# Performance work log

Measured on AMD Instinct MI355X. Metric: run time of the kernel, lower is better.

## Reference

```python
import jax, jax.numpy as jnp
import numpy as np

D = 768  # input_hidden_dim
H = 768  # TGLU_hidden_dim
E = 128  # num_entity
B = 32   # batch_size
S = 128  # max_seq_len
LN_EPS = 1e-5


def setup_inputs() -> dict:
    key = jax.random.key(0)
    ks = jax.random.split(key, 14)
    sc = 1.0 / np.sqrt(D)
    return {
        "entity_text_cls": jax.random.normal(ks[0], (E, D), jnp.float32),
        "entity_text_tokens": jax.random.normal(ks[1], (E, S, D), jnp.float32),
        "mention_text_cls": jax.random.normal(ks[2], (B, D), jnp.float32),
        "mention_text_tokens": jax.random.normal(ks[3], (B, S, D), jnp.float32),
        "Wq": jax.random.normal(ks[4], (D, H), jnp.float32) * sc,
        "bq": jax.random.normal(ks[5], (H,), jnp.float32) * 0.02,
        "Wk": jax.random.normal(ks[6], (D, H), jnp.float32) * sc,
        "bk": jax.random.normal(ks[7], (H,), jnp.float32) * 0.02,
        "Wv": jax.random.normal(ks[8], (D, H), jnp.float32) * sc,
        "bv": jax.random.normal(ks[9], (H,), jnp.float32) * 0.02,
        "Wc": jax.random.normal(ks[10], (D, H), jnp.float32) * sc,
        "bc": jax.random.normal(ks[11], (H,), jnp.float32) * 0.02,
        "ln_g": jnp.ones((H,), jnp.float32),
        "ln_b": jnp.zeros((H,), jnp.float32),
    }


def reference(entity_text_cls, entity_text_tokens, mention_text_cls, mention_text_tokens,
              Wq, bq, Wk, bk, Wv, bv, Wc, bc, ln_g, ln_b):
    # projections
    cls_fc = entity_text_cls @ Wc + bc                     # [E, H]
    q = entity_text_tokens @ Wq + bq                       # [E, S, H]
    k = mention_text_tokens @ Wk + bk                      # [B, S, H]
    v = mention_text_tokens @ Wv + bv                      # [B, S, H]
    # broadcast cross attention: every entity attends to every mention
    scale = 1.0 / jnp.sqrt(jnp.asarray(H, q.dtype))
    scores = jnp.einsum('esh,bth->ebst', q, k) * scale     # [E, B, S, S]
    probs = jax.nn.softmax(scores, axis=-1)                # [E, B, S, S]
    # context = mean over query positions of probs @ v  -> fuse mean into einsum
    seq = jnp.asarray(q.shape[1], q.dtype)
    ctx = jnp.einsum('ebst,bth->ebh', probs, v) / seq      # [E, B, H]
    # layernorm over H
    mu = jnp.mean(ctx, axis=-1, keepdims=True)
    var = jnp.mean(jnp.square(ctx - mu), axis=-1, keepdims=True)
    ctx_ln = (ctx - mu) * jax.lax.rsqrt(var + LN_EPS) * ln_g + ln_b
    # dual matching scores
    g2l = jnp.einsum('eh,ebh->eb', cls_fc, ctx_ln).T       # [B, E]
    g2g = mention_text_cls @ entity_text_cls.T             # [B, E]
    return (g2l + g2g) * 0.5
```

## Files before the change

### kernel.cpp

```cpp
#include <hip/hip_runtime.h>

typedef unsigned short u16;
typedef __bf16 bf16x8 __attribute__((ext_vector_type(8)));
typedef float f32x4 __attribute__((ext_vector_type(4)));
typedef u16 u16x8 __attribute__((ext_vector_type(8)));
typedef u16 u16x4 __attribute__((ext_vector_type(4)));

static __device__ __forceinline__ u16 f2bf(float x){
  unsigned u = __float_as_uint(x);
  u += 0x7fffu + ((u >> 16) & 1u);
  return (u16)(u >> 16);
}
static __device__ __forceinline__ float bf2f(u16 u){
  return __uint_as_float(((unsigned)u) << 16);
}

#define MFMA __builtin_amdgcn_mfma_f32_16x16x32_bf16

#define GLD1(GP, LP) __builtin_amdgcn_global_load_lds( \
    (const __attribute__((address_space(1))) unsigned int*)(GP), \
    (__attribute__((address_space(3))) unsigned int*)(LP), 16, 0, 0)

#define DECL_ACC \
  f32x4 acc00={},acc01={},acc02={},acc03={}, \
        acc10={},acc11={},acc12={},acc13={}, \
        acc20={},acc21={},acc22={},acc23={}, \
        acc30={},acc31={},acc32={},acc33={};

#define CORE_SETUP \
  int tid = threadIdx.x; \
  int lane = tid & 63, w = tid >> 6; \
  int wm = (w >> 1) * 64, wn = (w & 1) * 64; \
  int quad = lane >> 4, l16 = lane & 15; \
  int r8 = lane >> 3, c8 = lane & 7; \
  int p0 = quad ^ (l16 & 7); \
  const u16* Agl = Ablk + (size_t)(w*32 + r8)*KS + (size_t)((c8 ^ r8)*8); \
  const u16* Bgl = Bblk + (size_t)(w*32 + r8)*KS + (size_t)((c8 ^ r8)*8); \
  u16* sAl = sA + w*2048; \
  u16* sBl = sB + w*2048; \
  const u16* paA0 = sA + (wm + l16)*64 + p0*8; \
  const u16* paA1 = sA + (wm + l16)*64 + (p0^4)*8; \
  const u16* paB0 = sB + (wn + l16)*64 + p0*8; \
  const u16* paB1 = sB + (wn + l16)*64 + (p0^4)*8;

#define GLDS8(K0) do { \
  const u16* ga_ = Agl + (K0); \
  const u16* gb_ = Bgl + (K0); \
  GLD1(ga_,         sAl);        GLD1(ga_ +  8*KS, sAl +  512); \
  GLD1(ga_ + 16*KS, sAl + 1024); GLD1(ga_ + 24*KS, sAl + 1536); \
  GLD1(gb_,         sBl);        GLD1(gb_ +  8*KS, sBl +  512); \
  GLD1(gb_ + 16*KS, sBl + 1024); GLD1(gb_ + 24*KS, sBl + 1536); \
} while(0)

#define KKSTEP(PA, PB) do { \
  bf16x8 a0 = *(const bf16x8*)(PA); \
  bf16x8 a1 = *(const bf16x8*)((PA) + 1024); \
  bf16x8 a2 = *(const bf16x8*)((PA) + 2048); \
  bf16x8 a3 = *(const bf16x8*)((PA) + 3072); \
  bf16x8 b0 = *(const bf16x8*)(PB); \
  bf16x8 b1 = *(const bf16x8*)((PB) + 1024); \
  bf16x8 b2 = *(const bf16x8*)((PB) + 2048); \
  bf16x8 b3 = *(const bf16x8*)((PB) + 3072); \
  acc00 = MFMA(a0,b0,acc00,0,0,0); acc01 = MFMA(a0,b1,acc01,0,0,0); \
  acc02 = MFMA(a0,b2,acc02,0,0,0); acc03 = MFMA(a0,b3,acc03,0,0,0); \
  acc10 = MFMA(a1,b0,acc10,0,0,0); acc11 = MFMA(a1,b1,acc11,0,0,0); \
  acc12 = MFMA(a1,b2,acc12,0,0,0); acc13 = MFMA(a1,b3,acc13,0,0,0); \
  acc20 = MFMA(a2,b0,acc20,0,0,0); acc21 = MFMA(a2,b1,acc21,0,0,0); \
  acc22 = MFMA(a2,b2,acc22,0,0,0); acc23 = MFMA(a2,b3,acc23,0,0,0); \
  acc30 = MFMA(a3,b0,acc30,0,0,0); acc31 = MFMA(a3,b1,acc31,0,0,0); \
  acc32 = MFMA(a3,b2,acc32,0,0,0); acc33 = MFMA(a3,b3,acc33,0,0,0); \
} while(0)

#define KLOOP do { \
  for (int k0 = 0; k0 < KLEN; k0 += 64){ \
    __syncthreads(); \
    GLDS8(k0); \
    __syncthreads(); \
    KKSTEP(paA0, paB0); \
    KKSTEP(paA1, paB1); \
  } } while(0)

template<int KLEN, int KS, bool TRANSC>
static __device__ __forceinline__ void gemm128_core(
    const u16* __restrict__ Ablk, const u16* __restrict__ Bblk,
    const float* __restrict__ bias, u16* __restrict__ C,
    int mb, int nb, u16* sA, u16* sB)
{
  CORE_SETUP
  DECL_ACC
  KLOOP;
  int cb = nb*128 + wn + l16;
  float bb0=0.f, bb1=0.f, bb2=0.f, bb3=0.f;
  if (bias){ bb0=bias[cb]; bb1=bias[cb+16]; bb2=bias[cb+32]; bb3=bias[cb+48]; }
  if constexpr (!TRANSC) {
#define GEPI(IM,A0,A1,A2,A3) do { \
  int r0_ = mb*128 + wm + (IM)*16 + quad*4; \
  _Pragma("unroll") \
  for (int j=0;j<4;j++){ \
    C[(size_t)(r0_+j)*768 + cb     ] = f2bf(A0[j]+bb0); \
    C[(size_t)(r0_+j)*768 + cb + 16] = f2bf(A1[j]+bb1); \
    C[(size_t)(r0_+j)*768 + cb + 32] = f2bf(A2[j]+bb2); \
    C[(size_t)(r0_+j)*768 + cb + 48] = f2bf(A3[j]+bb3); \
  } } while(0)
    GEPI(0, acc00,acc01,acc02,acc03);
    GEPI(1, acc10,acc11,acc12,acc13);
    GEPI(2, acc20,acc21,acc22,acc23);
    GEPI(3, acc30,acc31,acc32,acc33);
#undef GEPI
  } else {
#define GEPT(IM,A0,A1,A2,A3) do { \
  int t0_ = wm + (IM)*16 + quad*4; \
  u16x4 p0_ = {f2bf(A0[0]+bb0),f2bf(A0[1]+bb0),f2bf(A0[2]+bb0),f2bf(A0[3]+bb0)}; \
  u16x4 p1_ = {f2bf(A1[0]+bb1),f2bf(A1[1]+bb1),f2bf(A1[2]+bb1),f2bf(A1[3]+bb1)}; \
  u16x4 p2_ = {f2bf(A2[0]+bb2),f2bf(A2[1]+bb2),f2bf(A2[2]+bb2),f2bf(A2[3]+bb2)}; \
  u16x4 p3_ = {f2bf(A3[0]+bb3),f2bf(A3[1]+bb3),f2bf(A3[2]+bb3),f2bf(A3[3]+bb3)}; \
  *(u16x4*)(C + (size_t)(cb     )*128 + t0_) = p0_; \
  *(u16x4*)(C + (size_t)(cb + 16)*128 + t0_) = p1_; \
  *(u16x4*)(C + (size_t)(cb + 32)*128 + t0_) = p2_; \
  *(u16x4*)(C + (size_t)(cb + 48)*128 + t0_) = p3_; \
} while(0)
    GEPT(0, acc00,acc01,acc02,acc03);
    GEPT(1, acc10,acc11,acc12,acc13);
    GEPT(2, acc20,acc21,acc22,acc23);
    GEPT(3, acc30,acc31,acc32,acc33);
#undef GEPT
  }
}

__global__ __launch_bounds__(256) void prep(
    const float* __restrict__ etok, u16* __restrict__ entb,
    const float* __restrict__ mtok, u16* __restrict__ menb,
    const float* __restrict__ ecls, u16* __restrict__ eclsb,
    const float* __restrict__ Wv, const float* __restrict__ Wc,
    u16* __restrict__ wvt, u16* __restrict__ wct,
    const float* __restrict__ Wq, const float* __restrict__ Wk,
    u16* __restrict__ mtb,
    const float* __restrict__ bq, const float* __restrict__ bk,
    float* __restrict__ wrb, float* __restrict__ c2b)
{
  __shared__ __align__(16) u16 shm[2*128*72];
  int blk = blockIdx.x;
  int tid = threadIdx.x;
  if (blk < 36){
    int mbq = blk/6, nbq = blk%6;
    u16* tA = shm; u16* tB = shm + 128*72;
    int lane = tid & 63, w = tid >> 6;
    int wm = (w >> 1) * 64, wn = (w & 1) * 64;
    int quad = lane >> 4, l16 = lane & 15;
    int sr = tid >> 3, sc = (tid & 7) * 8;
    const float* Ag = Wq + (size_t)(mbq*128+sr)*768 + sc;
    const float* Bg = Wk + (size_t)(nbq*128+sr)*768 + sc;
    u16* tAp = tA + sr*72 + sc;
    u16* tBp = tB + sr*72 + sc;
    DECL_ACC
    for (int k0=0;k0<768;k0+=64){
      __syncthreads();
#define STG(G) do { \
      float4 xa0=*(const float4*)(Ag+(G)*32*768+k0), xa1=*(const float4*)(Ag+(G)*32*768+k0+4); \
      float4 xb0=*(const float4*)(Bg+(G)*32*768+k0), xb1=*(const float4*)(Bg+(G)*32*768+k0+4); \
      u16x8 ra={f2bf(xa0.x),f2bf(xa0.y),f2bf(xa0.z),f2bf(xa0.w), \
                f2bf(xa1.x),f2bf(xa1.y),f2bf(xa1.z),f2bf(xa1.w)}; \
      u16x8 rb={f2bf(xb0.x),f2bf(xb0.y),f2bf(xb0.z),f2bf(xb0.w), \
                f2bf(xb1.x),f2bf(xb1.y),f2bf(xb1.z),f2bf(xb1.w)}; \
      *(u16x8*)(tAp+(G)*32*72)=ra; *(u16x8*)(tBp+(G)*32*72)=rb; \
      } while(0)
      STG(0); STG(1); STG(2); STG(3);
#undef STG
      __syncthreads();
#define KK72(KB) do { \
      const u16* pa_=tA+(wm+l16)*72+(KB)+quad*8; \
      const u16* pb_=tB+(wn+l16)*72+(KB)+quad*8; \
      bf16x8 a0=*(const bf16x8*)(pa_),      a1=*(const bf16x8*)(pa_+16*72); \
      bf16x8 a2=*(const bf16x8*)(pa_+32*72),a3=*(const bf16x8*)(pa_+48*72); \
      bf16x8 b0=*(const bf16x8*)(pb_),      b1=*(const bf16x8*)(pb_+16*72); \
      bf16x8 b2=*(const bf16x8*)(pb_+32*72),b3=*(const bf16x8*)(pb_+48*72); \
      acc00=MFMA(a0,b0,acc00,0,0,0); acc01=MFMA(a0,b1,acc01,0,0,0); \
      acc02=MFMA(a0,b2,acc02,0,0,0); acc03=MFMA(a0,b3,acc03,0,0,0); \
      acc10=MFMA(a1,b0,acc10,0,0,0); acc11=MFMA(a1,b1,acc11,0,0,0); \
      acc12=MFMA(a1,b2,acc12,0,0,0); acc13=MFMA(a1,b3,acc13,0,0,0); \
      acc20=MFMA(a2,b0,acc20,0,0,0); acc21=MFMA(a2,b1,acc21,0,0,0); \
      acc22=MFMA(a2,b2,acc22,0,0,0); acc23=MFMA(a2,b3,acc23,0,0,0); \
      acc30=MFMA(a3,b0,acc30,0,0,0); acc31=MFMA(a3,b1,acc31,0,0,0); \
      acc32=MFMA(a3,b2,acc32,0,0,0); acc33=MFMA(a3,b3,acc33,0,0,0); \
      } while(0)
      KK72(0); KK72(32);
#undef KK72
    }
    int cb = nbq*128 + wn + l16;
#define GEPM(IM,A0,A1,A2,A3) do { \
    int r0_ = mbq*128 + wm + (IM)*16 + quad*4; \
    _Pragma("unroll") \
    for (int j=0;j<4;j++){ \
      mtb[(size_t)(r0_+j)*768 + cb     ] = f2bf(A0[j]); \
      mtb[(size_t)(r0_+j)*768 + cb + 16] = f2bf(A1[j]); \
      mtb[(size_t)(r0_+j)*768 + cb + 32] = f2bf(A2[j]); \
      mtb[(size_t)(r0_+j)*768 + cb + 48] = f2bf(A3[j]); \
    } } while(0)
    GEPM(0, acc00,acc01,acc02,acc03);
    GEPM(1, acc10,acc11,acc12,acc13);
    GEPM(2, acc20,acc21,acc22,acc23);
    GEPM(3, acc30,acc31,acc32,acc33);
#undef GEPM
  } else if (blk < 48){
    int n = blk - 36;
    const float* M; const float* v; float* o;
    int j;
    if (n < 6){ M=Wk; v=bq; o=wrb; j=n; } else { M=Wq; v=bk; o=c2b; j=n-6; }
    int rr = tid >> 1, row = j*128 + rr;
    const float4* p = (const float4*)(M + (size_t)row*768 + (tid&1)*384);
    const float4* q = (const float4*)(v + (tid&1)*384);
    float s = 0.f;
    #pragma unroll 8
    for (int i=0;i<96;i++){
      float4 a=p[i], c=q[i];
      s += a.x*c.x + a.y*c.y + a.z*c.z + a.w*c.w;
    }
    s += __shfl_xor(s, 1);
    if (!(tid&1)) o[row] = s;
  } else if (blk == 48){
    float s = 0.f;
    for (int i=tid;i<768;i+=256) s += bk[i]*bq[i];
    #pragma unroll
    for (int d2=1; d2<64; d2<<=1) s += __shfl_xor(s,d2);
    float* red = (float*)shm;
    int lane = tid & 63, w = tid >> 6;
    if (lane==0) red[w]=s;
    __syncthreads();
    if (tid==0) wrb[768] = red[0]+red[1]+red[2]+red[3];
  } else if (blk < 7777){
    int i = (blk - 49) * 256 + tid;
    const float* s; u16* d; int off;
    if (i < 1572864)      { s=etok; d=entb; off=i; }
    else if (i < 1966080) { s=mtok; d=menb; off=i-1572864; }
    else                  { s=ecls; d=eclsb; off=i-1966080; }
    const float4* s4 = (const float4*)s;
    float4 a = s4[(size_t)off*2], b = s4[(size_t)off*2+1];
    u16x8 r;
    r[0]=f2bf(a.x); r[1]=f2bf(a.y); r[2]=f2bf(a.z); r[3]=f2bf(a.w);
    r[4]=f2bf(b.x); r[5]=f2bf(b.y); r[6]=f2bf(b.z); r[7]=f2bf(b.w);
    *(u16x8*)(d + (size_t)off*8) = r;
  } else {
    int n = blk - 7777;
    int z = n / 576, rem = n % 576;
    const float* s = z ? Wc : Wv;
    u16*         d = z ? wct : wvt;
    float* t = (float*)shm;
    int bx = (rem % 24) * 32, by = (rem / 24) * 32;
    int tx = tid & 31, ty = (tid >> 5) * 4;
    for (int i=0;i<4;i++)
      t[(ty+i)*33 + tx] = s[(size_t)(by+ty+i)*768 + bx+tx];
    __syncthreads();
    for (int i=0;i<4;i++)
      d[(size_t)(bx+ty+i)*768 + by+tx] = f2bf(t[tx*33 + ty+i]);
  }
}

__global__ __launch_bounds__(256, 1) void proj(
    const u16* __restrict__ men, const u16* __restrict__ eclsb,
    const u16* __restrict__ wvt, const u16* __restrict__ wct,
    const u16* __restrict__ mtb,
    const float* __restrict__ bv, const float* __restrict__ bc,
    const float* __restrict__ c2b, const float* __restrict__ wrb,
    u16* __restrict__ vtb, u16* __restrict__ gtb, u16* __restrict__ clsb,
    float* __restrict__ rbias)
{
  __shared__ __align__(16) u16 sA[128*64];
  __shared__ __align__(16) u16 sB[128*64];
  int y = blockIdx.y, mb = blockIdx.x;
  if (y < 6){
    gemm128_core<768,768,true>(men + (size_t)mb*128*768, wvt + (size_t)y*128*768,
                               bv, vtb + (size_t)mb*98304, mb, y, sA, sB);
  } else if (y < 12){
    gemm128_core<768,768,false>(men + (size_t)mb*128*768, mtb + (size_t)(y-6)*128*768,
                                c2b, gtb, mb, y-6, sA, sB);
  } else if (y == 12){
    if (mb >= 6) return;
    gemm128_core<768,768,false>(eclsb, wct + (size_t)mb*128*768, bc, clsb, 0, mb, sA, sB);
  } else {
    int tid = threadIdx.x;
    int rr = tid >> 1, row = mb*128 + rr;
    const u16* p = men + (size_t)row*768 + (tid&1)*384;
    const float* q = wrb + (tid&1)*384;
    float s = 0.f;
    #pragma unroll 8
    for (int i=0;i<48;i++){
      u16x8 v = *(const u16x8*)(p + i*8);
      s += bf2f(v[0])*q[i*8]   + bf2f(v[1])*q[i*8+1]
         + bf2f(v[2])*q[i*8+2] + bf2f(v[3])*q[i*8+3]
         + bf2f(v[4])*q[i*8+4] + bf2f(v[5])*q[i*8+5]
         + bf2f(v[6])*q[i*8+6] + bf2f(v[7])*q[i*8+7];
    }
    s += __shfl_xor(s, 1);
    if (!(tid&1)) rbias[row] = s + wrb[768];
  }
}

__global__ __launch_bounds__(256, 1) void attnk(
    const u16* __restrict__ ent, const u16* __restrict__ gt,
    const float* __restrict__ rbias, u16* __restrict__ ptbf)
{
  __shared__ __align__(16) u16 sA[128*64];
  __shared__ __align__(16) u16 sB[128*64];
  __shared__ float rbufA[256];
  __shared__ float rbufB[256];
  int bi = blockIdx.x;
  int b = bi >> 7, e = bi & 127;
  const u16* Ablk = ent + (size_t)e * 128 * 768;
  const u16* Bblk = gt  + (size_t)b * 128 * 768;
  constexpr int KS = 768;
  CORE_SETUP
  DECL_ACC
  int ph = (bi & 3) * 3;
  for (int it = 0; it < 12; it++){
    int kidx = it + ph; if (kidx >= 12) kidx -= 12;
    int k0 = kidx << 6;
    __syncthreads();
    GLDS8(k0);
    __syncthreads();
    KKSTEP(paA0, paB0);
    KKSTEP(paA1, paB1);
  }
  const float c1 = 0.036084391824351615f * 1.4426950408889634f;
  float rs0 = rbias[b*128 + wn      + l16] * c1;
  float rs1 = rbias[b*128 + wn + 16 + l16] * c1;
  float rs2 = rbias[b*128 + wn + 32 + l16] * c1;
  float rs3 = rbias[b*128 + wn + 48 + l16] * c1;
#define EXPSUM(IM,A0,A1,A2,A3) do { \
  _Pragma("unroll") \
  for (int j=0;j<4;j++){ \
    int r_ = wm + (IM)*16 + quad*4 + j; \
    float e0 = exp2f(fmaf(A0[j], c1, rs0)); \
    float e1 = exp2f(fmaf(A1[j], c1, rs1)); \
    float e2 = exp2f(fmaf(A2[j], c1, rs2)); \
    float e3 = exp2f(fmaf(A3[j], c1, rs3)); \
    A0[j]=e0; A1[j]=e1; A2[j]=e2; A3[j]=e3; \
    float s = (e0+e1)+(e2+e3); \
    s += __shfl_xor(s,1); s += __shfl_xor(s,2); \
    s += __shfl_xor(s,4); s += __shfl_xor(s,8); \
    if (l16==0) rbufB[(w&1)*128 + r_] = s; \
  } } while(0)
  EXPSUM(0, acc00,acc01,acc02,acc03);
  EXPSUM(1, acc10,acc11,acc12,acc13);
  EXPSUM(2, acc20,acc21,acc22,acc23);
  EXPSUM(3, acc30,acc31,acc32,acc33);
#undef EXPSUM
  __syncthreads();
  float csum0=0.f, csum1=0.f, csum2=0.f, csum3=0.f;
#define CSUM(IM,A0,A1,A2,A3) do { \
  _Pragma("unroll") \
  for (int j=0;j<4;j++){ \
    int r_ = wm + (IM)*16 + quad*4 + j; \
    float inv = __builtin_amdgcn_rcpf(rbufB[r_]+rbufB[128+r_]); \
    csum0 += A0[j]*inv; csum1 += A1[j]*inv; \
    csum2 += A2[j]*inv; csum3 += A3[j]*inv; \
  } } while(0)
  CSUM(0, acc00,acc01,acc02,acc03);
  CSUM(1, acc10,acc11,acc12,acc13);
  CSUM(2, acc20,acc21,acc22,acc23);
  CSUM(3, acc30,acc31,acc32,acc33);
#undef CSUM
  csum0 += __shfl_xor(csum0,16); csum0 += __shfl_xor(csum0,32);
  csum1 += __shfl_xor(csum1,16); csum1 += __shfl_xor(csum1,32);
  csum2 += __shfl_xor(csum2,16); csum2 += __shfl_xor(csum2,32);
  csum3 += __shfl_xor(csum3,16); csum3 += __shfl_xor(csum3,32);
  if (quad == 0){
    rbufA[(w>>1)*128 + wn      + l16] = csum0;
    rbufA[(w>>1)*128 + wn + 16 + l16] = csum1;
    rbufA[(w>>1)*128 + wn + 32 + l16] = csum2;
    rbufA[(w>>1)*128 + wn + 48 + l16] = csum3;
  }
  __syncthreads();
  if (tid < 128)
    ptbf[((size_t)b*128 + e)*128 + tid] =
        f2bf((rbufA[tid] + rbufA[128+tid]) * 0.0078125f);
}

__global__ __launch_bounds__(256, 1) void ctx2(
    const u16* __restrict__ ptbf, const u16* __restrict__ vtb,
    u16* __restrict__ ctxb)
{
  __shared__ __align__(16) u16 sA[128*64];
  __shared__ __align__(16) u16 sB[128*64];
  int b = blockIdx.y, nb = blockIdx.x;
  gemm128_core<128,128,false>(ptbf + (size_t)b*16384,
                              vtb + (size_t)b*98304 + (size_t)nb*16384,
                              nullptr, ctxb + (size_t)b*98304, 0, nb, sA, sB);
}

__global__ __launch_bounds__(256) void fin(
    const u16* __restrict__ ctxb, const u16* __restrict__ clsfc,
    const float* __restrict__ ecls, const float* __restrict__ mcls,
    const float* __restrict__ lng, const float* __restrict__ lnb,
    float* __restrict__ out)
{
  int bi = blockIdx.x;
  int b = bi >> 7, e = bi & 127;
  int tid = threadIdx.x;
  int lane = tid & 63, w = tid >> 6;
  __shared__ float redbuf[8];
  const u16* cr = ctxb + ((size_t)b*128 + e)*768;
  float a0 = bf2f(cr[tid]), a1 = bf2f(cr[tid+256]), a2 = bf2f(cr[tid+512]);
  float s1 = a0+a1+a2;
  float s2 = a0*a0 + a1*a1 + a2*a2;
  #pragma unroll
  for (int d2=1; d2<64; d2<<=1){ s1 += __shfl_xor(s1,d2); s2 += __shfl_xor(s2,d2); }
  if (lane==0){ redbuf[w]=s1; redbuf[4+w]=s2; }
  __syncthreads();
  s1 = redbuf[0]+redbuf[1]+redbuf[2]+redbuf[3];
  s2 = redbuf[4]+redbuf[5]+redbuf[6]+redbuf[7];
  float mu = s1 * (1.0f/768.0f);
  float var = s2 * (1.0f/768.0f) - mu*mu;
  float rstd = rsqrtf(var + 1e-5f);
  float dd = 0.f;
  {
    int h = tid;
    float y = (a0-mu)*rstd*lng[h] + lnb[h];
    dd += y * bf2f(clsfc[e*768+h]) + mcls[b*768+h]*ecls[e*768+h];
    h = tid + 256;
    y = (a1-mu)*rstd*lng[h] + lnb[h];
    dd += y * bf2f(clsfc[e*768+h]) + mcls[b*768+h]*ecls[e*768+h];
    h = tid + 512;
    y = (a2-mu)*rstd*lng[h] + lnb[h];
    dd += y * bf2f(clsfc[e*768+h]) + mcls[b*768+h]*ecls[e*768+h];
  }
  #pragma unroll
  for (int d2=1; d2<64; d2<<=1) dd += __shfl_xor(dd,d2);
  __syncthreads();
  if (lane==0) redbuf[w] = dd;
  __syncthreads();
  if (tid==0) out[bi] = 0.5f * (redbuf[0]+redbuf[1]+redbuf[2]+redbuf[3]);
}

extern "C" void kernel_launch(void* const* d_in, const int* in_sizes, int n_in,
                              void* d_out, int out_size, void* d_ws, size_t ws_size,
                              hipStream_t stream)
{
  (void)in_sizes; (void)n_in; (void)out_size; (void)ws_size;
  const float* ecls = (const float*)d_in[0];
  const float* etok = (const float*)d_in[1];
  const float* mcls = (const float*)d_in[2];
  const float* mtok = (const float*)d_in[3];
  const float* Wq   = (const float*)d_in[4];
  const float* bq   = (const float*)d_in[5];
  const float* Wk   = (const float*)d_in[6];
  const float* bk   = (const float*)d_in[7];
  const float* Wv   = (const float*)d_in[8];
  const float* bv   = (const float*)d_in[9];
  const float* Wc   = (const float*)d_in[10];
  const float* bc   = (const float*)d_in[11];
  const float* lng  = (const float*)d_in[12];
  const float* lnb  = (const float*)d_in[13];
  float* out = (float*)d_out;
  char* ws = (char*)d_ws;

  u16* ent_bf  = (u16*)(ws + 0);
  u16* men_bf  = (u16*)(ws + 25165824);
  u16* ecls_bf = (u16*)(ws + 31457280);
  u16* wvt     = (u16*)(ws + 31653888);
  u16* wct     = (u16*)(ws + 32833536);
  u16* mtb     = (u16*)(ws + 34013184);
  u16* vtb     = (u16*)(ws + 35192832);
  u16* clsb    = (u16*)(ws + 41484288);
  u16* gtb     = (u16*)(ws + 41680896);
  float* rbias = (float*)(ws + 47972352);
  float* wrb   = (float*)(ws + 47988736);
  float* c2b   = (float*)(ws + 47992832);
  u16* ptbf    = (u16*)(ws + 47996928);
  u16* ctxb    = (u16*)(ws + 49045504);

  prep<<<8929, 256, 0, stream>>>(etok, ent_bf, mtok, men_bf, ecls, ecls_bf,
                                 Wv, Wc, wvt, wct, Wq, Wk, mtb,
                                 bq, bk, wrb, c2b);
  proj<<<dim3(32,14), 256, 0, stream>>>(men_bf, ecls_bf, wvt, wct, mtb,
                                        bv, bc, c2b, wrb,
                                        vtb, gtb, clsb, rbias);
  attnk<<<4096, 256, 0, stream>>>(ent_bf, gtb, rbias, ptbf);
  ctx2<<<dim3(6,32), 256, 0, stream>>>(ptbf, vtb, ctxb);
  fin<<<4096, 256, 0, stream>>>(ctxb, clsb, ecls, mcls, lng, lnb, out);
}
```

Before: 299.1 us.

## Use FP8 operands and scaled MFMA for the attention score GEMM

Entity tokens and the folded query-key projection output are now stored as FP8 instead of bf16, and the score GEMM in the attention kernel uses the 16x16x128 FP8 scaled MFMA with 128-wide K tiles. This halves the bytes loaded for the dominant per-(entity, batch) GEMM and raises MFMA throughput per instruction. The cost is reduced precision in the softmax scores, which may affect accuracy against the reference, and the per-block K rotation phase is dropped.

```diff
diff --git a/kernel.cpp b/kernel.cpp
--- a/kernel.cpp
+++ b/kernel.cpp
@@ -1,10 +1,12 @@
 #include <hip/hip_runtime.h>
 
 typedef unsigned short u16;
+typedef unsigned char u8;
 typedef __bf16 bf16x8 __attribute__((ext_vector_type(8)));
 typedef float f32x4 __attribute__((ext_vector_type(4)));
 typedef u16 u16x8 __attribute__((ext_vector_type(8)));
 typedef u16 u16x4 __attribute__((ext_vector_type(4)));
+typedef int i32x8 __attribute__((ext_vector_type(8)));
 
 static __device__ __forceinline__ u16 f2bf(float x){
   unsigned u = __float_as_uint(x);
@@ -14,8 +16,14 @@
 static __device__ __forceinline__ float bf2f(u16 u){
   return __uint_as_float(((unsigned)u) << 16);
 }
+static __device__ __forceinline__ u8 f2fp8(float x){
+  int p = __builtin_amdgcn_cvt_pk_fp8_f32(x, x, 0, false);
+  return (u8)(p & 0xff);
+}
 
 #define MFMA __builtin_amdgcn_mfma_f32_16x16x32_bf16
+#define MFMA8(A,B,C) __builtin_amdgcn_mfma_scale_f32_16x16x128_f8f6f4( \
+    (A), (B), (C), 0, 0, 0, 0x7F7F7F7F, 0, 0x7F7F7F7F)
 
 #define GLD1(GP, LP) __builtin_amdgcn_global_load_lds( \
     (const __attribute__((address_space(1))) unsigned int*)(GP), \
@@ -80,10 +88,10 @@
     KKSTEP(paA1, paB1); \
   } } while(0)
 
-template<int KLEN, int KS, bool TRANSC>
+template<int KLEN, int KS, int OM>
 static __device__ __forceinline__ void gemm128_core(
     const u16* __restrict__ Ablk, const u16* __restrict__ Bblk,
-    const float* __restrict__ bias, u16* __restrict__ C,
+    const float* __restrict__ bias, void* __restrict__ Cv,
     int mb, int nb, u16* sA, u16* sB)
 {
   CORE_SETUP
@@ -92,7 +100,8 @@
   int cb = nb*128 + wn + l16;
   float bb0=0.f, bb1=0.f, bb2=0.f, bb3=0.f;
   if (bias){ bb0=bias[cb]; bb1=bias[cb+16]; bb2=bias[cb+32]; bb3=bias[cb+48]; }
-  if constexpr (!TRANSC) {
+  if constexpr (OM == 0) {
+    u16* C = (u16*)Cv;
 #define GEPI(IM,A0,A1,A2,A3) do { \
   int r0_ = mb*128 + wm + (IM)*16 + quad*4; \
   _Pragma("unroll") \
@@ -107,7 +116,8 @@
     GEPI(2, acc20,acc21,acc22,acc23);
     GEPI(3, acc30,acc31,acc32,acc33);
 #undef GEPI
-  } else {
+  } else if constexpr (OM == 1) {
+    u16* C = (u16*)Cv;
 #define GEPT(IM,A0,A1,A2,A3) do { \
   int t0_ = wm + (IM)*16 + quad*4; \
   u16x4 p0_ = {f2bf(A0[0]+bb0),f2bf(A0[1]+bb0),f2bf(A0[2]+bb0),f2bf(A0[3]+bb0)}; \
@@ -124,11 +134,27 @@
     GEPT(2, acc20,acc21,acc22,acc23);
     GEPT(3, acc30,acc31,acc32,acc33);
 #undef GEPT
+  } else {
+    u8* C = (u8*)Cv;
+#define GEP8(IM,A0,A1,A2,A3) do { \
+  int r0_ = mb*128 + wm + (IM)*16 + quad*4; \
+  _Pragma("unroll") \
+  for (int j=0;j<4;j++){ \
+    C[(size_t)(r0_+j)*768 + cb     ] = f2fp8(A0[j]+bb0); \
+    C[(size_t)(r0_+j)*768 + cb + 16] = f2fp8(A1[j]+bb1); \
+    C[(size_t)(r0_+j)*768 + cb + 32] = f2fp8(A2[j]+bb2); \
+    C[(size_t)(r0_+j)*768 + cb + 48] = f2fp8(A3[j]+bb3); \
+  } } while(0)
+    GEP8(0, acc00,acc01,acc02,acc03);
+    GEP8(1, acc10,acc11,acc12,acc13);
+    GEP8(2, acc20,acc21,acc22,acc23);
+    GEP8(3, acc30,acc31,acc32,acc33);
+#undef GEP8
   }
 }
 
 __global__ __launch_bounds__(256) void prep(
-    const float* __restrict__ etok, u16* __restrict__ entb,
+    const float* __restrict__ etok, u8* __restrict__ ent8,
     const float* __restrict__ mtok, u16* __restrict__ menb,
     const float* __restrict__ ecls, u16* __restrict__ eclsb,
     const float* __restrict__ Wv, const float* __restrict__ Wc,
@@ -229,16 +255,26 @@
     if (tid==0) wrb[768] = red[0]+red[1]+red[2]+red[3];
   } else if (blk < 7777){
     int i = (blk - 49) * 256 + tid;
-    const float* s; u16* d; int off;
-    if (i < 1572864)      { s=etok; d=entb; off=i; }
-    else if (i < 1966080) { s=mtok; d=menb; off=i-1572864; }
-    else                  { s=ecls; d=eclsb; off=i-1966080; }
-    const float4* s4 = (const float4*)s;
-    float4 a = s4[(size_t)off*2], b = s4[(size_t)off*2+1];
-    u16x8 r;
-    r[0]=f2bf(a.x); r[1]=f2bf(a.y); r[2]=f2bf(a.z); r[3]=f2bf(a.w);
-    r[4]=f2bf(b.x); r[5]=f2bf(b.y); r[6]=f2bf(b.z); r[7]=f2bf(b.w);
-    *(u16x8*)(d + (size_t)off*8) = r;
+    if (i < 1572864){
+      const float4* s4 = (const float4*)etok;
+      float4 a = s4[(size_t)i*2], b = s4[(size_t)i*2+1];
+      int d0 = __builtin_amdgcn_cvt_pk_fp8_f32(a.x, a.y, 0, false);
+      d0 = __builtin_amdgcn_cvt_pk_fp8_f32(a.z, a.w, d0, true);
+      int d1 = __builtin_amdgcn_cvt_pk_fp8_f32(b.x, b.y, 0, false);
+      d1 = __builtin_amdgcn_cvt_pk_fp8_f32(b.z, b.w, d1, true);
+      int2 r; r.x = d0; r.y = d1;
+      *(int2*)(ent8 + (size_t)i*8) = r;
+    } else {
+      const float* s; u16* d; int off;
+      if (i < 1966080) { s=mtok; d=menb; off=i-1572864; }
+      else             { s=ecls; d=eclsb; off=i-1966080; }
+      const float4* s4 = (const float4*)s;
+      float4 a = s4[(size_t)off*2], b = s4[(size_t)off*2+1];
+      u16x8 r;
+      r[0]=f2bf(a.x); r[1]=f2bf(a.y); r[2]=f2bf(a.z); r[3]=f2bf(a.w);
+      r[4]=f2bf(b.x); r[5]=f2bf(b.y); r[6]=f2bf(b.z); r[7]=f2bf(b.w);
+      *(u16x8*)(d + (size_t)off*8) = r;
+    }
   } else {
     int n = blk - 7777;
     int z = n / 576, rem = n % 576;
@@ -261,21 +297,21 @@
     const u16* __restrict__ mtb,
     const float* __restrict__ bv, const float* __restrict__ bc,
     const float* __restrict__ c2b, const float* __restrict__ wrb,
-    u16* __restrict__ vtb, u16* __restrict__ gtb, u16* __restrict__ clsb,
+    u16* __restrict__ vtb, u8* __restrict__ gt8, u16* __restrict__ clsb,
     float* __restrict__ rbias)
 {
   __shared__ __align__(16) u16 sA[128*64];
   __shared__ __align__(16) u16 sB[128*64];
   int y = blockIdx.y, mb = blockIdx.x;
   if (y < 6){
-    gemm128_core<768,768,true>(men + (size_t)mb*128*768, wvt + (size_t)y*128*768,
-                               bv, vtb + (size_t)mb*98304, mb, y, sA, sB);
+    gemm128_core<768,768,1>(men + (size_t)mb*128*768, wvt + (size_t)y*128*768,
+                            bv, vtb + (size_t)mb*98304, mb, y, sA, sB);
   } else if (y < 12){
-    gemm128_core<768,768,false>(men + (size_t)mb*128*768, mtb + (size_t)(y-6)*128*768,
-                                c2b, gtb, mb, y-6, sA, sB);
+    gemm128_core<768,768,2>(men + (size_t)mb*128*768, mtb + (size_t)(y-6)*128*768,
+                            c2b, gt8, mb, y-6, sA, sB);
   } else if (y == 12){
     if (mb >= 6) return;
-    gemm128_core<768,768,false>(eclsb, wct + (size_t)mb*128*768, bc, clsb, 0, mb, sA, sB);
+    gemm128_core<768,768,0>(eclsb, wct + (size_t)mb*128*768, bc, clsb, 0, mb, sA, sB);
   } else {
     int tid = threadIdx.x;
     int rr = tid >> 1, row = mb*128 + rr;
@@ -296,30 +332,73 @@
 }
 
 __global__ __launch_bounds__(256, 1) void attnk(
-    const u16* __restrict__ ent, const u16* __restrict__ gt,
+    const u8* __restrict__ ent, const u8* __restrict__ gt,
     const float* __restrict__ rbias, u16* __restrict__ ptbf)
 {
-  __shared__ __align__(16) u16 sA[128*64];
-  __shared__ __align__(16) u16 sB[128*64];
+  __shared__ __align__(16) u8 sA[128*128];
+  __shared__ __align__(16) u8 sB[128*128];
   __shared__ float rbufA[256];
   __shared__ float rbufB[256];
   int bi = blockIdx.x;
   int b = bi >> 7, e = bi & 127;
-  const u16* Ablk = ent + (size_t)e * 128 * 768;
-  const u16* Bblk = gt  + (size_t)b * 128 * 768;
-  constexpr int KS = 768;
-  CORE_SETUP
+  const u8* Ablk = ent + (size_t)e * 128 * 768;
+  const u8* Bblk = gt  + (size_t)b * 128 * 768;
+  int tid = threadIdx.x;
+  int lane = tid & 63, w = tid >> 6;
+  int wm = (w >> 1) * 64, wn = (w & 1) * 64;
+  int quad = lane >> 4, l16 = lane & 15;
+  int r8 = lane >> 3, c8 = lane & 7;
+  const u8* Agl = Ablk + (size_t)(w*32 + r8)*768 + (size_t)((c8 ^ r8)*16);
+  const u8* Bgl = Bblk + (size_t)(w*32 + r8)*768 + (size_t)((c8 ^ r8)*16);
+  u8* sAl = sA + w*4096;
+  u8* sBl = sB + w*4096;
+  int rb = l16 & 7;
+  const u8* paA0 = sA + (wm + l16)*128 + (((quad*2  )^rb)*16);
+  const u8* paA1 = sA + (wm + l16)*128 + (((quad*2+1)^rb)*16);
+  const u8* paB0 = sB + (wn + l16)*128 + (((quad*2  )^rb)*16);
+  const u8* paB1 = sB + (wn + l16)*128 + (((quad*2+1)^rb)*16);
   DECL_ACC
-  int ph = (bi & 3) * 3;
-  for (int it = 0; it < 12; it++){
-    int kidx = it + ph; if (kidx >= 12) kidx -= 12;
-    int k0 = kidx << 6;
+#define LDI(V, P0, P1) i32x8 V; { \
+  uint4 lo_ = *(const uint4*)(P0); uint4 hi_ = *(const uint4*)(P1); \
+  V = (i32x8){(int)lo_.x,(int)lo_.y,(int)lo_.z,(int)lo_.w, \
+              (int)hi_.x,(int)hi_.y,(int)hi_.z,(int)hi_.w}; }
+  for (int k0 = 0; k0 < 768; k0 += 128){
     __syncthreads();
-    GLDS8(k0);
+    {
+      const u8* ga_ = Agl + k0;
+      const u8* gb_ = Bgl + k0;
+      GLD1(ga_,          sAl);        GLD1(ga_ +  8*768, sAl + 1024);
+      GLD1(ga_ + 16*768, sAl + 2048); GLD1(ga_ + 24*768, sAl + 3072);
+      GLD1(gb_,          sBl);        GLD1(gb_ +  8*768, sBl + 1024);
+      GLD1(gb_ + 16*768, sBl + 2048); GLD1(gb_ + 24*768, sBl + 3072);
+    }
     __syncthreads();
-    KKSTEP(paA0, paB0);
-    KKSTEP(paA1, paB1);
+    LDI(b0, paB0,        paB1);
+    LDI(b1, paB0 + 2048, paB1 + 2048);
+    LDI(b2, paB0 + 4096, paB1 + 4096);
+    LDI(b3, paB0 + 6144, paB1 + 6144);
+    {
+      LDI(a_, paA0, paA1);
+      acc00=MFMA8(a_,b0,acc00); acc01=MFMA8(a_,b1,acc01);
+      acc02=MFMA8(a_,b2,acc02); acc03=MFMA8(a_,b3,acc03);
+    }
+    {
+      LDI(a_, paA0 + 2048, paA1 + 2048);
+      acc10=MFMA8(a_,b0,acc10); acc11=MFMA8(a_,b1,acc11);
+      acc12=MFMA8(a_,b2,acc12); acc13=MFMA8(a_,b3,acc13);
+    }
+    {
+      LDI(a_, paA0 + 4096, paA1 + 4096);
+      acc20=MFMA8(a_,b0,acc20); acc21=MFMA8(a_,b1,acc21);
+      acc22=MFMA8(a_,b2,acc22); acc23=MFMA8(a_,b3,acc23);
+    }
+    {
+      LDI(a_, paA0 + 6144, paA1 + 6144);
+      acc30=MFMA8(a_,b0,acc30); acc31=MFMA8(a_,b1,acc31);
+      acc32=MFMA8(a_,b2,acc32); acc33=MFMA8(a_,b3,acc33);
+    }
   }
+#undef LDI
   const float c1 = 0.036084391824351615f * 1.4426950408889634f;
   float rs0 = rbias[b*128 + wn      + l16] * c1;
   float rs1 = rbias[b*128 + wn + 16 + l16] * c1;
@@ -382,9 +461,9 @@
   __shared__ __align__(16) u16 sA[128*64];
   __shared__ __align__(16) u16 sB[128*64];
   int b = blockIdx.y, nb = blockIdx.x;
-  gemm128_core<128,128,false>(ptbf + (size_t)b*16384,
-                              vtb + (size_t)b*98304 + (size_t)nb*16384,
-                              nullptr, ctxb + (size_t)b*98304, 0, nb, sA, sB);
+  gemm128_core<128,128,0>(ptbf + (size_t)b*16384,
+                          vtb + (size_t)b*98304 + (size_t)nb*16384,
+                          nullptr, ctxb + (size_t)b*98304, 0, nb, sA, sB);
 }
 
 __global__ __launch_bounds__(256) void fin(
@@ -453,28 +532,28 @@
   float* out = (float*)d_out;
   char* ws = (char*)d_ws;
 
-  u16* ent_bf  = (u16*)(ws + 0);
-  u16* men_bf  = (u16*)(ws + 25165824);
-  u16* ecls_bf = (u16*)(ws + 31457280);
-  u16* wvt     = (u16*)(ws + 31653888);
-  u16* wct     = (u16*)(ws + 32833536);
-  u16* mtb     = (u16*)(ws + 34013184);
-  u16* vtb     = (u16*)(ws + 35192832);
-  u16* clsb    = (u16*)(ws + 41484288);
-  u16* gtb     = (u16*)(ws + 41680896);
-  float* rbias = (float*)(ws + 47972352);
-  float* wrb   = (float*)(ws + 47988736);
-  float* c2b   = (float*)(ws + 47992832);
-  u16* ptbf    = (u16*)(ws + 47996928);
-  u16* ctxb    = (u16*)(ws + 49045504);
-
-  prep<<<8929, 256, 0, stream>>>(etok, ent_bf, mtok, men_bf, ecls, ecls_bf,
+  u8*  ent8    = (u8*)(ws + 0);
+  u16* men_bf  = (u16*)(ws + 12582912);
+  u16* ecls_bf = (u16*)(ws + 18874368);
+  u16* wvt     = (u16*)(ws + 19070976);
+  u16* wct     = (u16*)(ws + 20250624);
+  u16* mtb     = (u16*)(ws + 21430272);
+  u16* vtb     = (u16*)(ws + 22609920);
+  u16* clsb    = (u16*)(ws + 28901376);
+  u8*  gt8     = (u8*)(ws + 29097984);
+  float* rbias = (float*)(ws + 32243712);
+  float* wrb   = (float*)(ws + 32260096);
+  float* c2b   = (float*)(ws + 32264192);
+  u16* ptbf    = (u16*)(ws + 32268288);
+  u16* ctxb    = (u16*)(ws + 33316864);
+
+  prep<<<8929, 256, 0, stream>>>(etok, ent8, mtok, men_bf, ecls, ecls_bf,
                                  Wv, Wc, wvt, wct, Wq, Wk, mtb,
                                  bq, bk, wrb, c2b);
   proj<<<dim3(32,14), 256, 0, stream>>>(men_bf, ecls_bf, wvt, wct, mtb,
                                         bv, bc, c2b, wrb,
-                                        vtb, gtb, clsb, rbias);
-  attnk<<<4096, 256, 0, stream>>>(ent_bf, gtb, rbias, ptbf);
+                                        vtb, gt8, clsb, rbias);
+  attnk<<<4096, 256, 0, stream>>>(ent8, gt8, rbias, ptbf);
   ctx2<<<dim3(6,32), 256, 0, stream>>>(ptbf, vtb, ctxb);
   fin<<<4096, 256, 0, stream>>>(ctxb, clsb, ecls, mcls, lng, lnb, out);
 }
```

After: 247.1 us. 17.4% less time.
